# Kernel optimization log

Hardware: AMD Instinct MI355X
Metric: run time of the kernel (lower is better)

The kernel has to match this reference:

```python
import jax, jax.numpy as jnp
from jax import lax
import numpy as np

B, T, D, H = 2048, 512, 16, 48


def _lstm_layer(x, W_ih, W_hh, b_ih, b_hh):
    """Single-layer LSTM, batch_first. x: [B,T,Din] -> hs: [B,T,H].
    PyTorch gate order: i, f, g, o."""
    h_dim = W_hh.shape[1]
    # Precompute input contribution for all timesteps: [B,T,4H]
    xg = jnp.einsum('btd,gd->btg', x, W_ih) + b_ih + b_hh
    xg = jnp.swapaxes(xg, 0, 1)  # [T,B,4H]

    def step(carry, xg_t):
        h, c = carry
        gates = xg_t + h @ W_hh.T  # [B,4H]
        i, f, g, o = jnp.split(gates, 4, axis=-1)
        i = jax.nn.sigmoid(i)
        f = jax.nn.sigmoid(f)
        g = jnp.tanh(g)
        o = jax.nn.sigmoid(o)
        c = f * c + i * g
        h = o * jnp.tanh(c)
        return (h, c), h

    bsz = x.shape[0]
    init = (jnp.zeros((bsz, h_dim), x.dtype), jnp.zeros((bsz, h_dim), x.dtype))
    _, hs = lax.scan(step, init, xg)
    return jnp.swapaxes(hs, 0, 1)  # [B,T,H]


def setup_inputs() -> dict:
    key = jax.random.key(0)
    ks = jax.random.split(key, 11)
    s_in = 1.0 / np.sqrt(H)
    return {
        'x': jax.random.normal(ks[0], (B, T, D), jnp.float32),
        'W_ih0': jax.random.normal(ks[1], (4 * H, D), jnp.float32) * s_in,
        'W_hh0': jax.random.normal(ks[2], (4 * H, H), jnp.float32) * s_in,
        'b_ih0': jax.random.normal(ks[3], (4 * H,), jnp.float32) * s_in,
        'b_hh0': jax.random.normal(ks[4], (4 * H,), jnp.float32) * s_in,
        'W_ih1': jax.random.normal(ks[5], (4 * H, H), jnp.float32) * s_in,
        'W_hh1': jax.random.normal(ks[6], (4 * H, H), jnp.float32) * s_in,
        'b_ih1': jax.random.normal(ks[7], (4 * H,), jnp.float32) * s_in,
        'b_hh1': jax.random.normal(ks[8], (4 * H,), jnp.float32) * s_in,
        'fc_w': jax.random.normal(ks[9], (1, H), jnp.float32) * s_in,
        'fc_b': jax.random.normal(ks[10], (1,), jnp.float32) * s_in,
    }


def reference(x, W_ih0, W_hh0, b_ih0, b_hh0, W_ih1, W_hh1, b_ih1, b_hh1, fc_w, fc_b):
    # 2-layer LSTM (eval mode: inter-layer dropout is identity)
    h1 = _lstm_layer(x, W_ih0, W_hh0, b_ih0, b_hh0)   # [B,T,H]
    h2 = _lstm_layer(h1, W_ih1, W_hh1, b_ih1, b_hh1)  # [B,T,H]
    last = h2[:, -1, :]                               # [B,H]
    logits = last @ fc_w.T + fc_b                     # [B,1]
    return jax.nn.sigmoid(logits)
```

## Files before the change

### kernel.cpp

```cpp
#include <hip/hip_runtime.h>

#define TT 512
#define DD 16
#define HH 48
#define BT 8
#define NTHR 768
#define CHUNK 64

#define XB 8192
#define STOT (XB + 1536)

typedef short bf8v __attribute__((ext_vector_type(8)));
typedef float f32x4 __attribute__((ext_vector_type(4)));

__device__ __forceinline__ ushort bfb(float f) {
    return __builtin_bit_cast(ushort, (__bf16)f);
}

__device__ __forceinline__ float sigf(float x) {
    float e = __builtin_amdgcn_exp2f(-1.4426950408889634f * x);
    return __builtin_amdgcn_rcpf(1.0f + e);
}

__device__ __forceinline__ void barrier_lds() {
    asm volatile("s_waitcnt lgkmcnt(0)\ns_barrier" ::: "memory");
}

__global__ __launch_bounds__(NTHR)
void lstm_kernel(const float* __restrict__ x,
                 const float* __restrict__ Wih0, const float* __restrict__ Whh0,
                 const float* __restrict__ bih0, const float* __restrict__ bhh0,
                 const float* __restrict__ Wih1, const float* __restrict__ Whh1,
                 const float* __restrict__ bih1, const float* __restrict__ bhh1,
                 const float* __restrict__ fcw, const float* __restrict__ fcb,
                 float* __restrict__ out)
{
    __shared__ alignas(16) ushort S[STOT];
    __shared__ float outl[BT][HH];

    const int tid  = threadIdx.x;
    const int lane = tid & 63;
    const int wave = tid >> 6;
    const int b0   = blockIdx.x * BT;

    const int colq = lane & 15;
    const int quad = lane >> 4;
    const int b    = colq & 7;
    const bool hi  = (colq >= 8);
    const int u    = wave * 4 + quad;

    const float L2E = 1.4426950408889634f;

    const int fbm = b * 8;
    const bool ringlane = (quad >= 2) && !hi;
    const int r0E = XB + quad * 64 + fbm;
    const int r0O = r0E + 768;
    const int r2E = XB + (8 + quad) * 64 + fbm;
    const int r2O = r2E + 768;
    const int r1statE = XB + (4 + quad) * 64 + fbm;
    const int r1statO = r1statE + 768;
    const int r1ring0 = (quad - 2) * 64 + colq * 8;
    const int inc = ringlane ? 256 : 0;
    const int kk = hi ? 48 + u : u;
    const int woff = (kk >> 3) * 64 + b * 8 + (kk & 7);
    const int wE = XB + 768 + woff;
    const int wO = XB + woff;

    const float fac = ((colq & 3) == 2) ? (-2.0f * L2E) : (-L2E);

    f32x4 bias0, bias1;
#pragma unroll
    for (int r = 0; r < 4; ++r) {
        float fr = (r == 2) ? (-2.0f * L2E) : (-L2E);
        bias0[r] = fr * (bih0[r * 48 + u] + bhh0[r * 48 + u]);
        bias1[r] = fr * (bih1[r * 48 + u] + bhh1[r * 48 + u]);
    }

    const int gi = (colq & 3) * 48 + wave * 4 + (colq >> 2);
    bf8v w0k0, w0k1, w1k0, w1k1, w1k2;
    {
        bf8v w;
#pragma unroll
        for (int j = 0; j < 8; ++j) {
            int k = quad * 8 + j;
            w[j] = (short)bfb(fac * Whh0[gi * 48 + k]);
        }
        w0k0 = w;
#pragma unroll
        for (int j = 0; j < 8; ++j) {
            int k = 32 + quad * 8 + j;
            float v = (k < 48) ? Whh0[gi * 48 + k] : Wih0[gi * 16 + (k - 48)];
            w[j] = (short)bfb(fac * v);
        }
        w0k1 = w;
#pragma unroll
        for (int j = 0; j < 8; ++j) {
            int k = quad * 8 + j;
            w[j] = (short)bfb(fac * Wih1[gi * 48 + k]);
        }
        w1k0 = w;
#pragma unroll
        for (int j = 0; j < 8; ++j) {
            int k = 32 + quad * 8 + j;
            float v = (k < 48) ? Wih1[gi * 48 + k] : Whh1[gi * 48 + (k - 48)];
            w[j] = (short)bfb(fac * v);
        }
        w1k1 = w;
#pragma unroll
        for (int j = 0; j < 8; ++j) {
            int k = 64 + quad * 8 + j;
            w[j] = (short)bfb(fac * Whh1[gi * 48 + (k - 48)]);
        }
        w1k2 = w;
    }

    const int g_  = tid & 3;
    const int bb_ = (tid >> 2) & 7;
    const int tlL = tid >> 5;
    const float* xpA = x + ((size_t)(b0 + bb_) * TT + tlL) * DD + g_ * 4;
    const float* xpB = xpA + 24 * DD;
    const int saA = tlL * 128 + (g_ >> 1) * 64 + bb_ * 8 + (g_ & 1) * 4;
    const int saB = saA + 24 * 128;
    float4 st0, st1;

#define STAGE(Hn) { \
        st0 = *(const float4*)(xpA + (Hn) * (32 * DD)); \
        if (tid < 256) st1 = *(const float4*)(xpB + (Hn) * (32 * DD)); \
    }
#define COMMIT(Hn) { \
        ushort4 s4; \
        s4.x = bfb(st0.x); s4.y = bfb(st0.y); s4.z = bfb(st0.z); s4.w = bfb(st0.w); \
        *(ushort4*)&S[saA + ((Hn) & 1) * 4096] = s4; \
        if (tid < 256) { \
            s4.x = bfb(st1.x); s4.y = bfb(st1.y); s4.z = bfb(st1.z); s4.w = bfb(st1.w); \
            *(ushort4*)&S[saB + ((Hn) & 1) * 4096] = s4; \
        } \
    }

    {
        uint* p = (uint*)S;
        for (int i = tid; i < STOT / 2; i += NTHR) p[i] = 0;
    }
    __syncthreads();

    STAGE(0)
    COMMIT(0)
    __syncthreads();
    STAGE(1)

    float c = 0.f;
    float hv = 0.f;

#define MFMA(A, B, C) __builtin_amdgcn_mfma_f32_16x16x32_bf16(A, B, C, 0, 0, 0)

#define BODY(V0A, V1A, V2A, WA, DOL1) { \
        bf8v v0 = *(const bf8v*)&S[V0A]; \
        bf8v v1 = *(const bf8v*)&S[V1A]; \
        bf8v v2 = *(const bf8v*)&S[V2A]; \
        f32x4 acc0 = MFMA(w0k0, v0, bias0); \
        acc0 = MFMA(w0k1, v1, acc0); \
        f32x4 pre; \
        if (DOL1) { \
            f32x4 acc1 = MFMA(w1k0, v0, bias1); \
            acc1 = MFMA(w1k1, v1, acc1); \
            acc1 = MFMA(w1k2, v2, acc1); \
            pre[0] = hi ? acc1[0] : acc0[0]; \
            pre[1] = hi ? acc1[1] : acc0[1]; \
            pre[2] = hi ? acc1[2] : acc0[2]; \
            pre[3] = hi ? acc1[3] : acc0[3]; \
        } else { \
            pre = acc0; \
        } \
        float ei = __builtin_amdgcn_exp2f(pre[0]); \
        float ef = __builtin_amdgcn_exp2f(pre[1]); \
        float eg = __builtin_amdgcn_exp2f(pre[2]); \
        float eo = __builtin_amdgcn_exp2f(pre[3]); \
        float P = (1.0f + ei) * (1.0f + eg); \
        float Q = 1.0f + ef; \
        float R = __builtin_amdgcn_rcpf(P * Q); \
        float cn = R * __builtin_fmaf(P, c, (1.0f - eg) * Q); \
        if (!DOL1) cn = hi ? c : cn;    \
        c = cn; \
        float ec = __builtin_amdgcn_exp2f(-2.0f * L2E * cn); \
        float roc = __builtin_amdgcn_rcpf((1.0f + eo) * (1.0f + ec)); \
        hv = (1.0f - ec) * roc; \
        ushort hb = bfb(hv); \
        if (!hi) { S[WA] = hb; } \
        else if (DOL1) { S[WA] = hb; } \
        barrier_lds(); \
    }

    int r1E = 0, r1O = 0;
    for (int H = 0; H < 16; ++H) {
        if ((H & 1) == 0) {
            r1E = ringlane ? r1ring0 : r1statE;
            r1O = ringlane ? (128 + r1ring0) : r1statO;
        }
        int p0 = 0;
        if (H == 0) {
            BODY(r0E, r1E, r2E, wE, false)
            BODY(r0O, r1O, r2O, wO, true)
            r1E += inc; r1O += inc;
            p0 = 1;
        }
        for (int p = p0; p < 16; ++p) {
            BODY(r0E, r1E, r2E, wE, true)
            BODY(r0O, r1O, r2O, wO, true)
            r1E += inc; r1O += inc;
        }
        if (H < 15) {
            COMMIT(H + 1)
            __syncthreads();
            if (H < 14) STAGE(H + 2)
        }
    }

    {
        int r1p = ringlane ? (r1ring0 + 32 * 256) : r1statE;
        bf8v v0 = *(const bf8v*)&S[r0E];
        bf8v v1 = *(const bf8v*)&S[r1p];
        bf8v v2 = *(const bf8v*)&S[r2E];
        f32x4 acc1 = MFMA(w1k0, v0, bias1);
        acc1 = MFMA(w1k1, v1, acc1);
        acc1 = MFMA(w1k2, v2, acc1);
        float ei = __builtin_amdgcn_exp2f(acc1[0]);
        float ef = __builtin_amdgcn_exp2f(acc1[1]);
        float eg = __builtin_amdgcn_exp2f(acc1[2]);
        float eo = __builtin_amdgcn_exp2f(acc1[3]);
        float P = (1.0f + ei) * (1.0f + eg);
        float Q = 1.0f + ef;
        float R = __builtin_amdgcn_rcpf(P * Q);
        float cn = R * __builtin_fmaf(P, c, (1.0f - eg) * Q);
        float ec = __builtin_amdgcn_exp2f(-2.0f * L2E * cn);
        float roc = __builtin_amdgcn_rcpf((1.0f + eo) * (1.0f + ec));
        hv = (1.0f - ec) * roc;
    }

    if (hi) outl[b][u] = hv;
    __syncthreads();
    if (tid < BT) {
        float s = fcb[0];
        for (int uu = 0; uu < HH; ++uu) s = __builtin_fmaf(outl[tid][uu], fcw[uu], s);
        out[b0 + tid] = sigf(s);
    }
#undef BODY
#undef MFMA
#undef STAGE
#undef COMMIT
}

extern "C" void kernel_launch(void* const* d_in, const int* in_sizes, int n_in,
                              void* d_out, int out_size, void* d_ws, size_t ws_size,
                              hipStream_t stream) {
    const float* x    = (const float*)d_in[0];
    const float* Wih0 = (const float*)d_in[1];
    const float* Whh0 = (const float*)d_in[2];
    const float* bih0 = (const float*)d_in[3];
    const float* bhh0 = (const float*)d_in[4];
    const float* Wih1 = (const float*)d_in[5];
    const float* Whh1 = (const float*)d_in[6];
    const float* bih1 = (const float*)d_in[7];
    const float* bhh1 = (const float*)d_in[8];
    const float* fcw  = (const float*)d_in[9];
    const float* fcb  = (const float*)d_in[10];
    lstm_kernel<<<2048 / BT, NTHR, 0, stream>>>(x, Wih0, Whh0, bih0, bhh0,
                                                Wih1, Whh1, bih1, bhh1, fcw, fcb,
                                                (float*)d_out);
}
```

Measured before the change: 269.5 us.

## Cut block to 4 waves, each handling three hidden-unit tiles

Shrinks the workgroup from 12 waves to 4 and gives each wave three 16-gate tiles (NT=3), keeping weights, biases and cell states for all three in registers. The x staging loop now loads four float4 per thread instead of one or two. The goal is cheaper per-timestep barriers with fewer waves and more independent MFMA/transcendental work per wave to hide latency. In exchange each wave carries more serial work and registers per step, and with 256 blocks of 4 waves the GPU is less occupied.

```diff
diff --git a/kernel.cpp b/kernel.cpp
--- a/kernel.cpp
+++ b/kernel.cpp
@@ -4,7 +4,8 @@
 #define DD 16
 #define HH 48
 #define BT 8
-#define NTHR 768
+#define NTHR 256
+#define NT 3
 #define CHUNK 64
 
 #define XB 8192
@@ -26,7 +27,7 @@
     asm volatile("s_waitcnt lgkmcnt(0)\ns_barrier" ::: "memory");
 }
 
-__global__ __launch_bounds__(NTHR)
+__global__ __launch_bounds__(NTHR, 1)
 void lstm_kernel(const float* __restrict__ x,
                  const float* __restrict__ Wih0, const float* __restrict__ Whh0,
                  const float* __restrict__ bih0, const float* __restrict__ bhh0,
@@ -47,7 +48,7 @@
     const int quad = lane >> 4;
     const int b    = colq & 7;
     const bool hi  = (colq >= 8);
-    const int u    = wave * 4 + quad;
+    const int u0   = wave * 4 + quad;
 
     const float L2E = 1.4426950408889634f;
 
@@ -61,79 +62,83 @@
     const int r1statO = r1statE + 768;
     const int r1ring0 = (quad - 2) * 64 + colq * 8;
     const int inc = ringlane ? 256 : 0;
-    const int kk = hi ? 48 + u : u;
-    const int woff = (kk >> 3) * 64 + b * 8 + (kk & 7);
+    const int kk0 = hi ? 48 + u0 : u0;
+    const int woff = (kk0 >> 3) * 64 + b * 8 + (kk0 & 7);
     const int wE = XB + 768 + woff;
     const int wO = XB + woff;
 
     const float fac = ((colq & 3) == 2) ? (-2.0f * L2E) : (-L2E);
 
-    f32x4 bias0, bias1;
-#pragma unroll
-    for (int r = 0; r < 4; ++r) {
-        float fr = (r == 2) ? (-2.0f * L2E) : (-L2E);
-        bias0[r] = fr * (bih0[r * 48 + u] + bhh0[r * 48 + u]);
-        bias1[r] = fr * (bih1[r * 48 + u] + bhh1[r * 48 + u]);
-    }
-
-    const int gi = (colq & 3) * 48 + wave * 4 + (colq >> 2);
-    bf8v w0k0, w0k1, w1k0, w1k1, w1k2;
-    {
+    f32x4 bias0[NT], bias1[NT];
+#pragma unroll
+    for (int i = 0; i < NT; ++i) {
+        const int ui = u0 + 16 * i;
+#pragma unroll
+        for (int r = 0; r < 4; ++r) {
+            float fr = (r == 2) ? (-2.0f * L2E) : (-L2E);
+            bias0[i][r] = fr * (bih0[r * 48 + ui] + bhh0[r * 48 + ui]);
+            bias1[i][r] = fr * (bih1[r * 48 + ui] + bhh1[r * 48 + ui]);
+        }
+    }
+
+    bf8v w0k0[NT], w0k1[NT], w1k0[NT], w1k1[NT], w1k2[NT];
+#pragma unroll
+    for (int i = 0; i < NT; ++i) {
+        const int gi = (colq & 3) * 48 + wave * 4 + 16 * i + (colq >> 2);
         bf8v w;
 #pragma unroll
         for (int j = 0; j < 8; ++j) {
             int k = quad * 8 + j;
             w[j] = (short)bfb(fac * Whh0[gi * 48 + k]);
         }
-        w0k0 = w;
+        w0k0[i] = w;
 #pragma unroll
         for (int j = 0; j < 8; ++j) {
             int k = 32 + quad * 8 + j;
             float v = (k < 48) ? Whh0[gi * 48 + k] : Wih0[gi * 16 + (k - 48)];
             w[j] = (short)bfb(fac * v);
         }
-        w0k1 = w;
+        w0k1[i] = w;
 #pragma unroll
         for (int j = 0; j < 8; ++j) {
             int k = quad * 8 + j;
             w[j] = (short)bfb(fac * Wih1[gi * 48 + k]);
         }
-        w1k0 = w;
+        w1k0[i] = w;
 #pragma unroll
         for (int j = 0; j < 8; ++j) {
             int k = 32 + quad * 8 + j;
             float v = (k < 48) ? Wih1[gi * 48 + k] : Whh1[gi * 48 + (k - 48)];
             w[j] = (short)bfb(fac * v);
         }
-        w1k1 = w;
+        w1k1[i] = w;
 #pragma unroll
         for (int j = 0; j < 8; ++j) {
             int k = 64 + quad * 8 + j;
             w[j] = (short)bfb(fac * Whh1[gi * 48 + (k - 48)]);
         }
-        w1k2 = w;
+        w1k2[i] = w;
     }
 
     const int g_  = tid & 3;
     const int bb_ = (tid >> 2) & 7;
-    const int tlL = tid >> 5;
-    const float* xpA = x + ((size_t)(b0 + bb_) * TT + tlL) * DD + g_ * 4;
-    const float* xpB = xpA + 24 * DD;
-    const int saA = tlL * 128 + (g_ >> 1) * 64 + bb_ * 8 + (g_ & 1) * 4;
-    const int saB = saA + 24 * 128;
-    float4 st0, st1;
+    const int tl0 = tid >> 5;
+    const float* xp = x + ((size_t)(b0 + bb_) * TT + tl0) * DD + g_ * 4;
+    const int sa = tl0 * 128 + (g_ >> 1) * 64 + bb_ * 8 + (g_ & 1) * 4;
+    float4 st[4];
 
 #define STAGE(Hn) { \
-        st0 = *(const float4*)(xpA + (Hn) * (32 * DD)); \
-        if (tid < 256) st1 = *(const float4*)(xpB + (Hn) * (32 * DD)); \
+        _Pragma("unroll") \
+        for (int j = 0; j < 4; ++j) \
+            st[j] = *(const float4*)(xp + (Hn) * (32 * DD) + j * (8 * DD)); \
     }
 #define COMMIT(Hn) { \
-        ushort4 s4; \
-        s4.x = bfb(st0.x); s4.y = bfb(st0.y); s4.z = bfb(st0.z); s4.w = bfb(st0.w); \
-        *(ushort4*)&S[saA + ((Hn) & 1) * 4096] = s4; \
-        if (tid < 256) { \
-            s4.x = bfb(st1.x); s4.y = bfb(st1.y); s4.z = bfb(st1.z); s4.w = bfb(st1.w); \
-            *(ushort4*)&S[saB + ((Hn) & 1) * 4096] = s4; \
+        _Pragma("unroll") \
+        for (int j = 0; j < 4; ++j) { \
+            ushort4 s4; \
+            s4.x = bfb(st[j].x); s4.y = bfb(st[j].y); \
+            s4.z = bfb(st[j].z); s4.w = bfb(st[j].w); \
+            *(ushort4*)&S[sa + j * 1024 + ((Hn) & 1) * 4096] = s4; \
         } \
     }
 
@@ -148,8 +153,7 @@
     __syncthreads();
     STAGE(1)
 
-    float c = 0.f;
-    float hv = 0.f;
+    float c[NT] = {0.f, 0.f, 0.f};
 
 #define MFMA(A, B, C) __builtin_amdgcn_mfma_f32_16x16x32_bf16(A, B, C, 0, 0, 0)
 
@@ -157,36 +161,39 @@
         bf8v v0 = *(const bf8v*)&S[V0A]; \
         bf8v v1 = *(const bf8v*)&S[V1A]; \
         bf8v v2 = *(const bf8v*)&S[V2A]; \
-        f32x4 acc0 = MFMA(w0k0, v0, bias0); \
-        acc0 = MFMA(w0k1, v1, acc0); \
-        f32x4 pre; \
-        if (DOL1) { \
-            f32x4 acc1 = MFMA(w1k0, v0, bias1); \
-            acc1 = MFMA(w1k1, v1, acc1); \
-            acc1 = MFMA(w1k2, v2, acc1); \
-            pre[0] = hi ? acc1[0] : acc0[0]; \
-            pre[1] = hi ? acc1[1] : acc0[1]; \
-            pre[2] = hi ? acc1[2] : acc0[2]; \
-            pre[3] = hi ? acc1[3] : acc0[3]; \
-        } else { \
-            pre = acc0; \
+        _Pragma("unroll") \
+        for (int i = 0; i < NT; ++i) { \
+            f32x4 acc0 = MFMA(w0k0[i], v0, bias0[i]); \
+            acc0 = MFMA(w0k1[i], v1, acc0); \
+            f32x4 pre; \
+            if (DOL1) { \
+                f32x4 acc1 = MFMA(w1k0[i], v0, bias1[i]); \
+                acc1 = MFMA(w1k1[i], v1, acc1); \
+                acc1 = MFMA(w1k2[i], v2, acc1); \
+                pre[0] = hi ? acc1[0] : acc0[0]; \
+                pre[1] = hi ? acc1[1] : acc0[1]; \
+                pre[2] = hi ? acc1[2] : acc0[2]; \
+                pre[3] = hi ? acc1[3] : acc0[3]; \
+            } else { \
+                pre = acc0; \
+            } \
+            float ei = __builtin_amdgcn_exp2f(pre[0]); \
+            float ef = __builtin_amdgcn_exp2f(pre[1]); \
+            float eg = __builtin_amdgcn_exp2f(pre[2]); \
+            float eo = __builtin_amdgcn_exp2f(pre[3]); \
+            float P = (1.0f + ei) * (1.0f + eg); \
+            float Q = 1.0f + ef; \
+            float R = __builtin_amdgcn_rcpf(P * Q); \
+            float cn = R * __builtin_fmaf(P, c[i], (1.0f - eg) * Q); \
+            if (!DOL1) cn = hi ? c[i] : cn;    \
+            c[i] = cn; \
+            float ec = __builtin_amdgcn_exp2f(-2.0f * L2E * cn); \
+            float roc = __builtin_amdgcn_rcpf((1.0f + eo) * (1.0f + ec)); \
+            float h_ = (1.0f - ec) * roc; \
+            ushort hb = bfb(h_); \
+            if (!hi) { S[(WA) + i * 128] = hb; } \
+            else if (DOL1) { S[(WA) + i * 128] = hb; } \
         } \
-        float ei = __builtin_amdgcn_exp2f(pre[0]); \
-        float ef = __builtin_amdgcn_exp2f(pre[1]); \
-        float eg = __builtin_amdgcn_exp2f(pre[2]); \
-        float eo = __builtin_amdgcn_exp2f(pre[3]); \
-        float P = (1.0f + ei) * (1.0f + eg); \
-        float Q = 1.0f + ef; \
-        float R = __builtin_amdgcn_rcpf(P * Q); \
-        float cn = R * __builtin_fmaf(P, c, (1.0f - eg) * Q); \
-        if (!DOL1) cn = hi ? c : cn;    \
-        c = cn; \
-        float ec = __builtin_amdgcn_exp2f(-2.0f * L2E * cn); \
-        float roc = __builtin_amdgcn_rcpf((1.0f + eo) * (1.0f + ec)); \
-        hv = (1.0f - ec) * roc; \
-        ushort hb = bfb(hv); \
-        if (!hi) { S[WA] = hb; } \
-        else if (DOL1) { S[WA] = hb; } \
         barrier_lds(); \
     }
 
@@ -220,23 +227,25 @@
         bf8v v0 = *(const bf8v*)&S[r0E];
         bf8v v1 = *(const bf8v*)&S[r1p];
         bf8v v2 = *(const bf8v*)&S[r2E];
-        f32x4 acc1 = MFMA(w1k0, v0, bias1);
-        acc1 = MFMA(w1k1, v1, acc1);
-        acc1 = MFMA(w1k2, v2, acc1);
-        float ei = __builtin_amdgcn_exp2f(acc1[0]);
-        float ef = __builtin_amdgcn_exp2f(acc1[1]);
-        float eg = __builtin_amdgcn_exp2f(acc1[2]);
-        float eo = __builtin_amdgcn_exp2f(acc1[3]);
-        float P = (1.0f + ei) * (1.0f + eg);
-        float Q = 1.0f + ef;
-        float R = __builtin_amdgcn_rcpf(P * Q);
-        float cn = R * __builtin_fmaf(P, c, (1.0f - eg) * Q);
-        float ec = __builtin_amdgcn_exp2f(-2.0f * L2E * cn);
-        float roc = __builtin_amdgcn_rcpf((1.0f + eo) * (1.0f + ec));
-        hv = (1.0f - ec) * roc;
-    }
-
-    if (hi) outl[b][u] = hv;
+#pragma unroll
+        for (int i = 0; i < NT; ++i) {
+            f32x4 acc1 = MFMA(w1k0[i], v0, bias1[i]);
+            acc1 = MFMA(w1k1[i], v1, acc1);
+            acc1 = MFMA(w1k2[i], v2, acc1);
+            float ei = __builtin_amdgcn_exp2f(acc1[0]);
+            float ef = __builtin_amdgcn_exp2f(acc1[1]);
+            float eg = __builtin_amdgcn_exp2f(acc1[2]);
+            float eo = __builtin_amdgcn_exp2f(acc1[3]);
+            float P = (1.0f + ei) * (1.0f + eg);
+            float Q = 1.0f + ef;
+            float R = __builtin_amdgcn_rcpf(P * Q);
+            float cn = R * __builtin_fmaf(P, c[i], (1.0f - eg) * Q);
+            float ec = __builtin_amdgcn_exp2f(-2.0f * L2E * cn);
+            float roc = __builtin_amdgcn_rcpf((1.0f + eo) * (1.0f + ec));
+            float h_ = (1.0f - ec) * roc;
+            if (hi) outl[b][u0 + 16 * i] = h_;
+        }
+    }
     __syncthreads();
     if (tid < BT) {
         float s = fcb[0];
```

Measured after the change: 322.1 us. 1.2x slower.

## Fold commit into last step barrier and prescale cell state

Applied to the files above, without the earlier changes.

The cell state is now kept prescaled by -2·log2(e), which removes one multiply from the serial recurrence. The h store is made unconditional, so the hi lanes also write on the first step. The chunk COMMIT now runs inside the final timestep's body ahead of its LDS barrier, replacing the separate __syncthreads between chunks. This removes one full block barrier per chunk from the critical path. The risk is a race if that LDS barrier alone does not order the committed data for the next chunk's reads, and the unconditional store may write values that were previously suppressed.

```diff
diff --git a/kernel.cpp b/kernel.cpp
--- a/kernel.cpp
+++ b/kernel.cpp
@@ -50,6 +50,7 @@
     const int u    = wave * 4 + quad;
 
     const float L2E = 1.4426950408889634f;
+    const float K2  = -2.0f * L2E;
 
     const int fbm = b * 8;
     const bool ringlane = (quad >= 2) && !hi;
@@ -66,12 +67,12 @@
     const int wE = XB + 768 + woff;
     const int wO = XB + woff;
 
-    const float fac = ((colq & 3) == 2) ? (-2.0f * L2E) : (-L2E);
+    const float fac = ((colq & 3) == 2) ? K2 : (-L2E);
 
     f32x4 bias0, bias1;
 #pragma unroll
     for (int r = 0; r < 4; ++r) {
-        float fr = (r == 2) ? (-2.0f * L2E) : (-L2E);
+        float fr = (r == 2) ? K2 : (-L2E);
         bias0[r] = fr * (bih0[r * 48 + u] + bhh0[r * 48 + u]);
         bias1[r] = fr * (bih1[r * 48 + u] + bhh1[r * 48 + u]);
     }
@@ -153,7 +154,7 @@
 
 #define MFMA(A, B, C) __builtin_amdgcn_mfma_f32_16x16x32_bf16(A, B, C, 0, 0, 0)
 
-#define BODY(V0A, V1A, V2A, WA, DOL1) { \
+#define BODY(V0A, V1A, V2A, WA, DOL1, EXTRA) { \
         bf8v v0 = *(const bf8v*)&S[V0A]; \
         bf8v v1 = *(const bf8v*)&S[V1A]; \
         bf8v v2 = *(const bf8v*)&S[V2A]; \
@@ -177,18 +178,20 @@
         float eo = __builtin_amdgcn_exp2f(pre[3]); \
         float P = (1.0f + ei) * (1.0f + eg); \
         float Q = 1.0f + ef; \
+        float opo = 1.0f + eo; \
         float R = __builtin_amdgcn_rcpf(P * Q); \
-        float cn = R * __builtin_fmaf(P, c, (1.0f - eg) * Q); \
-        if (!DOL1) cn = hi ? c : cn;    \
-        c = cn; \
-        float ec = __builtin_amdgcn_exp2f(-2.0f * L2E * cn); \
-        float roc = __builtin_amdgcn_rcpf((1.0f + eo) * (1.0f + ec)); \
+        float kg = __builtin_fmaf(-K2, eg, K2);  \
+        float cs = R * __builtin_fmaf(P, c, kg * Q); \
+        if (!DOL1) cs = hi ? c : cs;    \
+        c = cs; \
+        float ec = __builtin_amdgcn_exp2f(cs); \
+        float roc = __builtin_amdgcn_rcpf(opo * (1.0f + ec)); \
         hv = (1.0f - ec) * roc; \
-        ushort hb = bfb(hv); \
-        if (!hi) { S[WA] = hb; } \
-        else if (DOL1) { S[WA] = hb; } \
+        S[WA] = bfb(hv); \
+        EXTRA \
         barrier_lds(); \
     }
+#define NOP_
 
     int r1E = 0, r1O = 0;
     for (int H = 0; H < 16; ++H) {
@@ -198,20 +201,24 @@
         }
         int p0 = 0;
         if (H == 0) {
-            BODY(r0E, r1E, r2E, wE, false)
-            BODY(r0O, r1O, r2O, wO, true)
+            BODY(r0E, r1E, r2E, wE, false, NOP_)
+            BODY(r0O, r1O, r2O, wO, true, NOP_)
             r1E += inc; r1O += inc;
             p0 = 1;
         }
-        for (int p = p0; p < 16; ++p) {
-            BODY(r0E, r1E, r2E, wE, true)
-            BODY(r0O, r1O, r2O, wO, true)
+        for (int p = p0; p < 15; ++p) {
+            BODY(r0E, r1E, r2E, wE, true, NOP_)
+            BODY(r0O, r1O, r2O, wO, true, NOP_)
             r1E += inc; r1O += inc;
         }
         if (H < 15) {
-            COMMIT(H + 1)
-            __syncthreads();
+            BODY(r0E, r1E, r2E, wE, true, NOP_)
+            BODY(r0O, r1O, r2O, wO, true, COMMIT(H + 1))
+            r1E += inc; r1O += inc;
             if (H < 14) STAGE(H + 2)
+        } else {
+            BODY(r0E, r1E, r2E, wE, true, NOP_)
+            BODY(r0O, r1O, r2O, wO, true, NOP_)
         }
     }
 
@@ -230,8 +237,9 @@
         float P = (1.0f + ei) * (1.0f + eg);
         float Q = 1.0f + ef;
         float R = __builtin_amdgcn_rcpf(P * Q);
-        float cn = R * __builtin_fmaf(P, c, (1.0f - eg) * Q);
-        float ec = __builtin_amdgcn_exp2f(-2.0f * L2E * cn);
+        float kg = __builtin_fmaf(-K2, eg, K2);
+        float cs = R * __builtin_fmaf(P, c, kg * Q);
+        float ec = __builtin_amdgcn_exp2f(cs);
         float roc = __builtin_amdgcn_rcpf((1.0f + eo) * (1.0f + ec));
         hv = (1.0f - ec) * roc;
     }
@@ -244,6 +252,7 @@
         out[b0 + tid] = sigf(s);
     }
 #undef BODY
+#undef NOP_
 #undef MFMA
 #undef STAGE
 #undef COMMIT
```

Result: no change. 274.4 us (median of 2 runs) (+1.8%).
